# Kernel tuning notes

Hardware: AMD Instinct MI355X
Metric: run time of the kernel (lower is better)

Reference implementation:

```python
import jax, jax.numpy as jnp
import numpy as np


def setup_inputs() -> dict:
    key = jax.random.key(0)
    B, N, D = 32, 1024, 1024
    x = jax.random.normal(key, (B, N, D), dtype=jnp.float32)
    return {"x": x}


def reference(x) -> jnp.ndarray:
    # query = key = value = x (the module's Linear layers are unused).
    # kl_divs[b,i,j] = KL(softmax(x[b,i]) || softmax(x[b,j])) for i != j, 0 on diag.
    # Since KL(p||p) == 0, the full vectorized KL matrix matches the looped version.
    logp = jax.nn.log_softmax(x, axis=-1)          # [B, N, D]
    p = jnp.exp(logp)                               # softmax(x)
    neg_ent = jnp.sum(p * logp, axis=-1)            # [B, N]  = sum p log p
    cross = jnp.einsum('bid,bjd->bij', p, logp)     # [B, N, N] = sum_d p_i log q_j
    kl = neg_ent[:, :, None] - cross                # [B, N, N]
    attn = jax.nn.softmax(-kl, axis=-1)             # [B, N, N]
    out = jnp.einsum('bij,bjd->bid', attn, x)       # value = x
    return out
```

## Files before the change

### kernel.cpp

```cpp
#include <hip/hip_runtime.h>
#include <hip/hip_bf16.h>
#include <stdint.h>

#define B_ 32
#define N_ 1024
#define D_ 1024

typedef __bf16 bf16x8 __attribute__((ext_vector_type(8)));
typedef float f32x4 __attribute__((ext_vector_type(4)));

static __device__ __forceinline__ unsigned short f2bf(float f) {
    union { float f; unsigned u; } v; v.f = f;
    unsigned r = v.u + 0x7fffu + ((v.u >> 16) & 1u);
    return (unsigned short)(r >> 16);
}

static __device__ __forceinline__ void gld_lds16(const void* g, void* l) {
    __builtin_amdgcn_global_load_lds(
        (const __attribute__((address_space(1))) void*)g,
        (__attribute__((address_space(3))) void*)l, 16, 0, 0);
}

__global__ __launch_bounds__(256) void prep_kernel(const float* __restrict__ x,
        unsigned short* __restrict__ pb, unsigned short* __restrict__ xb,
        float* __restrict__ lse) {
    int row  = blockIdx.x * 4 + (threadIdx.x >> 6);
    int lane = threadIdx.x & 63;
    const float4* xr = (const float4*)(x + (size_t)row * D_);

    float4 v[4];
    #pragma unroll
    for (int q = 0; q < 4; q++) v[q] = xr[lane + 64 * q];

    float m = -1e30f;
    #pragma unroll
    for (int q = 0; q < 4; q++)
        m = fmaxf(m, fmaxf(fmaxf(v[q].x, v[q].y), fmaxf(v[q].z, v[q].w)));
    #pragma unroll
    for (int o = 1; o < 64; o <<= 1) m = fmaxf(m, __shfl_xor(m, o, 64));

    float4 e[4];
    float s = 0.0f;
    #pragma unroll
    for (int q = 0; q < 4; q++) {
        e[q].x = __expf(v[q].x - m); e[q].y = __expf(v[q].y - m);
        e[q].z = __expf(v[q].z - m); e[q].w = __expf(v[q].w - m);
        s += e[q].x + e[q].y + e[q].z + e[q].w;
    }
    #pragma unroll
    for (int o = 1; o < 64; o <<= 1) s += __shfl_xor(s, o, 64);
    float inv = 1.0f / s;

    ushort4* pr = (ushort4*)(pb + (size_t)row * D_);
    ushort4* xw = (ushort4*)(xb + (size_t)row * D_);
    #pragma unroll
    for (int q = 0; q < 4; q++) {
        ushort4 pu, xu;
        pu.x = f2bf(e[q].x * inv); pu.y = f2bf(e[q].y * inv);
        pu.z = f2bf(e[q].z * inv); pu.w = f2bf(e[q].w * inv);
        xu.x = f2bf(v[q].x); xu.y = f2bf(v[q].y);
        xu.z = f2bf(v[q].z); xu.w = f2bf(v[q].w);
        pr[lane + 64 * q] = pu;
        xw[lane + 64 * q] = xu;
    }
    if (lane == 0) lse[row] = m + logf(s);
}

template<int MODE>
__global__ __launch_bounds__(512) void gemm_bt(const unsigned short* __restrict__ Ag,
        const unsigned short* __restrict__ Bg, void* __restrict__ Cg,
        const float* __restrict__ lse, float* __restrict__ rowsum) {
    const int K = 1024;
    int b = blockIdx.z;
    const unsigned short* A  = Ag + (size_t)b * N_ * K;
    const unsigned short* Bm = Bg + (size_t)b * N_ * K;
    int m0 = blockIdx.y * 256, n0 = blockIdx.x * 256;

    __shared__ unsigned short lds[32768];

    int t = threadIdx.x;
    int wave = t >> 6, lane = t & 63;
    int wr = wave >> 2, wc = wave & 3;
    int fm = lane & 15, gf = lane >> 4;
    int rsw = (fm >> 1) & 3;

    f32x4 acc[8][4];
    #pragma unroll
    for (int i = 0; i < 8; i++)
        #pragma unroll
        for (int j = 0; j < 4; j++)
            #pragma unroll
            for (int r = 0; r < 4; r++) acc[i][j][r] = 0.0f;

    int rr = t >> 2, s = t & 3;
    int sg = s ^ ((rr >> 1) & 3);
    int rbase = rr + (rr & 64);

    auto stage = [&](int g) {
        int tg = g >> 1, qg = g & 1, bg = tg & 1;
        int row = qg * 64 + rbase;
        const unsigned short* sa = A  + (size_t)(m0 + row) * K + tg * 32 + sg * 8;
        const unsigned short* sb = Bm + (size_t)(n0 + row) * K + tg * 32 + sg * 8;
        gld_lds16(sa, &lds[bg * 8192 + row * 32 + s * 8]);
        gld_lds16(sb, &lds[16384 + bg * 8192 + row * 32 + s * 8]);
    };

    stage(0); stage(1); stage(2);
    asm volatile("s_waitcnt vmcnt(2)" ::: "memory");
    __builtin_amdgcn_s_barrier();

    for (int tt = 0; tt < 32; ++tt) {
        int bb = tt & 1;
        const unsigned short* LA = &lds[bb * 8192];
        const unsigned short* LB = &lds[16384 + bb * 8192];
        bf16x8 bv[4];
        #pragma unroll
        for (int q = 0; q < 2; ++q) {
            if (q == 0) {
                #pragma unroll
                for (int j = 0; j < 4; ++j) {
                    int row = wc * 64 + j * 16 + fm;
                    bv[j] = *(const bf16x8*)&LB[row * 32 + (gf ^ rsw) * 8];
                }
            }
            bf16x8 av[4];
            #pragma unroll
            for (int i2 = 0; i2 < 4; ++i2) {
                int row = wr * 128 + (q * 4 + i2) * 16 + fm;
                av[i2] = *(const bf16x8*)&LA[row * 32 + (gf ^ rsw) * 8];
            }
            int g = 2 * tt + q + 3;
            if (g < 64) stage(g);

            __builtin_amdgcn_s_barrier();
            asm volatile("s_waitcnt lgkmcnt(0)" ::: "memory");
            __builtin_amdgcn_sched_barrier(0);
            __builtin_amdgcn_s_setprio(1);
            #pragma unroll
            for (int i2 = 0; i2 < 4; ++i2)
                #pragma unroll
                for (int j = 0; j < 4; ++j)
                    acc[q * 4 + i2][j] = __builtin_amdgcn_mfma_f32_16x16x32_bf16(
                        av[i2], bv[j], acc[q * 4 + i2][j], 0, 0, 0);
            __builtin_amdgcn_s_setprio(0);
            if (q == 1) {
                if (tt < 30)       asm volatile("s_waitcnt vmcnt(2)" ::: "memory");
                else if (tt == 30) asm volatile("s_waitcnt vmcnt(0)" ::: "memory");
            }
            __builtin_amdgcn_s_barrier();
        }
    }

    int cr = (lane >> 4) * 4;
    int cc = lane & 15;

    if (MODE == 0) {
        unsigned short* Co = (unsigned short*)Cg + (size_t)b * (size_t)N_ * N_;
        float lsev[4];
        #pragma unroll
        for (int j = 0; j < 4; j++) lsev[j] = lse[b * N_ + n0 + wc * 64 + j * 16 + cc];
        float rsum[32];
        #pragma unroll
        for (int q = 0; q < 32; q++) rsum[q] = 0.0f;
        #pragma unroll
        for (int i = 0; i < 8; i++) {
            #pragma unroll
            for (int r = 0; r < 4; r++) {
                int row = m0 + wr * 128 + i * 16 + cr + r;
                size_t ro = (size_t)row * N_;
                #pragma unroll
                for (int j = 0; j < 4; j++) {
                    int col = n0 + wc * 64 + j * 16 + cc;
                    float ev = __expf(acc[i][j][r] - lsev[j]);
                    unsigned short eb = f2bf(ev);
                    union { unsigned u; float f; } bk; bk.u = ((unsigned)eb) << 16;
                    Co[ro + col] = eb;
                    rsum[i * 4 + r] += bk.f;
                }
            }
        }
        #pragma unroll
        for (int q = 0; q < 32; q++) {
            float sv = rsum[q];
            sv += __shfl_xor(sv, 1, 64);
            sv += __shfl_xor(sv, 2, 64);
            sv += __shfl_xor(sv, 4, 64);
            sv += __shfl_xor(sv, 8, 64);
            rsum[q] = sv;
        }
        if (cc == 0) {
            #pragma unroll
            for (int q = 0; q < 32; q++) {
                int row = m0 + wr * 128 + (q >> 2) * 16 + cr + (q & 3);
                atomicAdd(&rowsum[b * N_ + row], rsum[q]);
            }
        }
    } else {
        float* Co = (float*)Cg + (size_t)b * (size_t)N_ * N_;
        #pragma unroll
        for (int i = 0; i < 8; i++) {
            #pragma unroll
            for (int r = 0; r < 4; r++) {
                int row = m0 + wr * 128 + i * 16 + cr + r;
                float inv = 1.0f / rowsum[b * N_ + row];
                size_t ro = (size_t)row * N_;
                #pragma unroll
                for (int j = 0; j < 4; j++) {
                    int col = n0 + wc * 64 + j * 16 + cc;
                    Co[ro + col] = acc[i][j][r] * inv;
                }
            }
        }
    }
}

__global__ __launch_bounds__(256) void transpose_kernel(const unsigned short* __restrict__ in,
        unsigned short* __restrict__ out) {
    int b  = blockIdx.z;
    int j0 = blockIdx.y * 64;
    int d0 = blockIdx.x * 64;
    __shared__ unsigned short tile[64][66];
    const unsigned short* ip = in + ((size_t)b * N_ + j0) * D_ + d0;
    int t = threadIdx.x;
    #pragma unroll
    for (int c = t; c < 512; c += 256) {
        int r = c >> 3, col = (c & 7) * 8;
        uint4 val = *(const uint4*)(ip + (size_t)r * D_ + col);
        unsigned int* dst = (unsigned int*)&tile[r][col];
        dst[0] = val.x; dst[1] = val.y; dst[2] = val.z; dst[3] = val.w;
    }
    __syncthreads();
    unsigned short* op = out + ((size_t)b * D_ + d0) * N_ + j0;
    #pragma unroll
    for (int c = t; c < 512; c += 256) {
        int r = c >> 3, col = (c & 7) * 8;
        unsigned short vals[8];
        #pragma unroll
        for (int k = 0; k < 8; k++) vals[k] = tile[col + k][r];
        uint4 o;
        o.x = (unsigned)vals[0] | ((unsigned)vals[1] << 16);
        o.y = (unsigned)vals[2] | ((unsigned)vals[3] << 16);
        o.z = (unsigned)vals[4] | ((unsigned)vals[5] << 16);
        o.w = (unsigned)vals[6] | ((unsigned)vals[7] << 16);
        *(uint4*)(op + (size_t)r * N_ + col) = o;
    }
}

extern "C" void kernel_launch(void* const* d_in, const int* in_sizes, int n_in,
                              void* d_out, int out_size, void* d_ws, size_t ws_size,
                              hipStream_t stream) {
    const float* x = (const float*)d_in[0];
    float* out = (float*)d_out;
    char* ws = (char*)d_ws;

    unsigned short* pb    = (unsigned short*)(ws);
    unsigned short* xb    = (unsigned short*)(ws + 67108864ULL);
    unsigned short* xbT   = (unsigned short*)(ws + 134217728ULL);
    unsigned short* attnE = (unsigned short*)(ws + 201326592ULL);
    float*          lse   = (float*)(ws + 268435456ULL);
    float*          rowsum= (float*)(ws + 268566528ULL);

    hipMemsetAsync(rowsum, 0, B_ * N_ * sizeof(float), stream);
    prep_kernel<<<dim3(B_ * N_ / 4), 256, 0, stream>>>(x, pb, xb, lse);
    transpose_kernel<<<dim3(16, 16, B_), 256, 0, stream>>>(xb, xbT);
    gemm_bt<0><<<dim3(4, 4, B_), 512, 0, stream>>>(pb, xb, attnE, lse, rowsum);
    gemm_bt<1><<<dim3(4, 4, B_), 512, 0, stream>>>(attnE, xbT, out, nullptr, rowsum);
}
```

Before: 428.0 us.

## Triple-buffer LDS and software-pipeline fragment loads in batched GEMM

Restructures the GEMM main loop into a 3-stage LDS ring buffer using 96KB of dynamic shared memory. LDS fragment reads for the next k-step are issued between MFMA groups, with register double-buffering. The kernel now needs only one barrier per k-step instead of two. Launch bounds request 2 blocks per CU, which caps register usage and may cause spills, and 96KB LDS per block may prevent two blocks from fitting on a CU.

```diff
diff --git a/kernel.cpp b/kernel.cpp
--- a/kernel.cpp
+++ b/kernel.cpp
@@ -66,8 +66,46 @@
     if (lane == 0) lse[row] = m + logf(s);
 }
 
+#define SB0() __builtin_amdgcn_sched_barrier(0)
+
+#define STEP(tt, bvC, a0C, bvN, a0N)                                            \
+  {                                                                             \
+    int brN = (brC == 2) ? 0 : brC + 1;                                         \
+    int bw  = (brN == 2) ? 0 : brN + 1;                                         \
+    asm volatile("s_waitcnt lgkmcnt(4)" ::: "memory");                          \
+    SB0();                                                                      \
+    __builtin_amdgcn_s_setprio(1);                                              \
+    _Pragma("unroll") for (int i2 = 0; i2 < 4; ++i2)                            \
+    _Pragma("unroll") for (int j = 0; j < 4; ++j)                               \
+      acc[i2][j] = __builtin_amdgcn_mfma_f32_16x16x32_bf16(a0C[i2], bvC[j],     \
+                                                           acc[i2][j], 0, 0, 0);\
+    __builtin_amdgcn_s_setprio(0);                                              \
+    if ((tt) + 2 < 32) stage(bw, (tt) + 2);                                     \
+    asm volatile("s_waitcnt lgkmcnt(0)" ::: "memory");                          \
+    if ((tt) < 30)        asm volatile("s_waitcnt vmcnt(4)" ::: "memory");      \
+    else if ((tt) == 30)  asm volatile("s_waitcnt vmcnt(0)" ::: "memory");      \
+    SB0();                                                                      \
+    __builtin_amdgcn_s_barrier();                                               \
+    SB0();                                                                      \
+    if ((tt) + 1 < 32) {                                                        \
+      _Pragma("unroll") for (int j = 0; j < 4; ++j)  bvN[j]  = lB(brN, j);      \
+      _Pragma("unroll") for (int i2 = 0; i2 < 4; ++i2) a0N[i2] = lA(brN, 0, i2);\
+    }                                                                           \
+    SB0();                                                                      \
+    __builtin_amdgcn_s_setprio(1);                                              \
+    _Pragma("unroll") for (int i2 = 0; i2 < 4; ++i2)                            \
+    _Pragma("unroll") for (int j = 0; j < 4; ++j)                               \
+      acc[4 + i2][j] = __builtin_amdgcn_mfma_f32_16x16x32_bf16(a1[i2], bvC[j],  \
+                                                        acc[4 + i2][j], 0, 0, 0);\
+    __builtin_amdgcn_s_setprio(0);                                              \
+    if ((tt) + 1 < 32) {                                                        \
+      _Pragma("unroll") for (int i2 = 0; i2 < 4; ++i2) a1[i2] = lA(brN, 1, i2); \
+    }                                                                           \
+    brC = brN;                                                                  \
+  }
+
 template<int MODE>
-__global__ __launch_bounds__(512) void gemm_bt(const unsigned short* __restrict__ Ag,
+__global__ __launch_bounds__(512, 2) void gemm_bt(const unsigned short* __restrict__ Ag,
         const unsigned short* __restrict__ Bg, void* __restrict__ Cg,
         const float* __restrict__ lse, float* __restrict__ rowsum) {
     const int K = 1024;
@@ -76,13 +114,12 @@
     const unsigned short* Bm = Bg + (size_t)b * N_ * K;
     int m0 = blockIdx.y * 256, n0 = blockIdx.x * 256;
 
-    __shared__ unsigned short lds[32768];
+    extern __shared__ char lds[];
 
     int t = threadIdx.x;
     int wave = t >> 6, lane = t & 63;
     int wr = wave >> 2, wc = wave & 3;
     int fm = lane & 15, gf = lane >> 4;
-    int rsw = (fm >> 1) & 3;
 
     f32x4 acc[8][4];
     #pragma unroll
@@ -95,60 +132,54 @@
     int rr = t >> 2, s = t & 3;
     int sg = s ^ ((rr >> 1) & 3);
     int rbase = rr + (rr & 64);
-
-    auto stage = [&](int g) {
-        int tg = g >> 1, qg = g & 1, bg = tg & 1;
-        int row = qg * 64 + rbase;
-        const unsigned short* sa = A  + (size_t)(m0 + row) * K + tg * 32 + sg * 8;
-        const unsigned short* sb = Bm + (size_t)(n0 + row) * K + tg * 32 + sg * 8;
-        gld_lds16(sa, &lds[bg * 8192 + row * 32 + s * 8]);
-        gld_lds16(sb, &lds[16384 + bg * 8192 + row * 32 + s * 8]);
+    int row0s = rbase;
+    int row1s = 64 + rbase;
+    const unsigned short* pA0 = A  + (size_t)(m0 + row0s) * K + sg * 8;
+    const unsigned short* pA1 = A  + (size_t)(m0 + row1s) * K + sg * 8;
+    const unsigned short* pB0 = Bm + (size_t)(n0 + row0s) * K + sg * 8;
+    const unsigned short* pB1 = Bm + (size_t)(n0 + row1s) * K + sg * 8;
+    int dA0 = row0s * 64 + s * 16;
+    int dA1 = row1s * 64 + s * 16;
+
+    auto stage = [&](int bw, int tg) {
+        char* ab = lds + bw * 16384;
+        char* bb = lds + 49152 + bw * 16384;
+        gld_lds16(pA0 + tg * 32, ab + dA0);
+        gld_lds16(pA1 + tg * 32, ab + dA1);
+        gld_lds16(pB0 + tg * 32, bb + dA0);
+        gld_lds16(pB1 + tg * 32, bb + dA1);
     };
 
-    stage(0); stage(1); stage(2);
-    asm volatile("s_waitcnt vmcnt(2)" ::: "memory");
+    int slot = (gf ^ ((fm >> 1) & 3)) * 16;
+    int arow = wr * 128 + fm;
+    int brow = wc * 64 + fm;
+
+    auto lA = [&](int br, int q, int i2) {
+        return *(const bf16x8*)(lds + br * 16384 + (arow + q * 64 + i2 * 16) * 64 + slot);
+    };
+    auto lB = [&](int br, int j) {
+        return *(const bf16x8*)(lds + 49152 + br * 16384 + (brow + j * 16) * 64 + slot);
+    };
+
+    bf16x8 bvA[4], a0A[4], bvB[4], a0B[4], a1[4];
+
+    stage(0, 0);
+    stage(1, 1);
+    asm volatile("s_waitcnt vmcnt(4)" ::: "memory");
     __builtin_amdgcn_s_barrier();
-
-    for (int tt = 0; tt < 32; ++tt) {
-        int bb = tt & 1;
-        const unsigned short* LA = &lds[bb * 8192];
-        const unsigned short* LB = &lds[16384 + bb * 8192];
-        bf16x8 bv[4];
-        #pragma unroll
-        for (int q = 0; q < 2; ++q) {
-            if (q == 0) {
-                #pragma unroll
-                for (int j = 0; j < 4; ++j) {
-                    int row = wc * 64 + j * 16 + fm;
-                    bv[j] = *(const bf16x8*)&LB[row * 32 + (gf ^ rsw) * 8];
-                }
-            }
-            bf16x8 av[4];
-            #pragma unroll
-            for (int i2 = 0; i2 < 4; ++i2) {
-                int row = wr * 128 + (q * 4 + i2) * 16 + fm;
-                av[i2] = *(const bf16x8*)&LA[row * 32 + (gf ^ rsw) * 8];
-            }
-            int g = 2 * tt + q + 3;
-            if (g < 64) stage(g);
-
-            __builtin_amdgcn_s_barrier();
-            asm volatile("s_waitcnt lgkmcnt(0)" ::: "memory");
-            __builtin_amdgcn_sched_barrier(0);
-            __builtin_amdgcn_s_setprio(1);
-            #pragma unroll
-            for (int i2 = 0; i2 < 4; ++i2)
-                #pragma unroll
-                for (int j = 0; j < 4; ++j)
-                    acc[q * 4 + i2][j] = __builtin_amdgcn_mfma_f32_16x16x32_bf16(
-                        av[i2], bv[j], acc[q * 4 + i2][j], 0, 0, 0);
-            __builtin_amdgcn_s_setprio(0);
-            if (q == 1) {
-                if (tt < 30)       asm volatile("s_waitcnt vmcnt(2)" ::: "memory");
-                else if (tt == 30) asm volatile("s_waitcnt vmcnt(0)" ::: "memory");
-            }
-            __builtin_amdgcn_s_barrier();
-        }
+    SB0();
+    #pragma unroll
+    for (int j = 0; j < 4; ++j)  bvA[j]  = lB(0, j);
+    #pragma unroll
+    for (int i2 = 0; i2 < 4; ++i2) a0A[i2] = lA(0, 0, i2);
+    SB0();
+    #pragma unroll
+    for (int i2 = 0; i2 < 4; ++i2) a1[i2] = lA(0, 1, i2);
+
+    int brC = 0;
+    for (int tp = 0; tp < 16; ++tp) {
+        STEP(2 * tp,     bvA, a0A, bvB, a0B);
+        STEP(2 * tp + 1, bvB, a0B, bvA, a0A);
     }
 
     int cr = (lane >> 4) * 4;
@@ -263,6 +294,6 @@
     hipMemsetAsync(rowsum, 0, B_ * N_ * sizeof(float), stream);
     prep_kernel<<<dim3(B_ * N_ / 4), 256, 0, stream>>>(x, pb, xb, lse);
     transpose_kernel<<<dim3(16, 16, B_), 256, 0, stream>>>(xb, xbT);
-    gemm_bt<0><<<dim3(4, 4, B_), 512, 0, stream>>>(pb, xb, attnE, lse, rowsum);
-    gemm_bt<1><<<dim3(4, 4, B_), 512, 0, stream>>>(attnE, xbT, out, nullptr, rowsum);
-}
+    gemm_bt<0><<<dim3(4, 4, B_), 512, 98304, stream>>>(pb, xb, attnE, lse, rowsum);
+    gemm_bt<1><<<dim3(4, 4, B_), 512, 98304, stream>>>(attnE, xbT, out, nullptr, rowsum);
+}
```

Result: no change. 420.3 us (-1.8%).
